# Kernel optimization log

Hardware: AMD Instinct MI355X
Metric: run time of the kernel (lower is better)

## Reference

```python
import jax, jax.numpy as jnp
import numpy as np

ANNEALING_SCALE = 0.1
BS, NV, S, D, V = 2, 16, 1024, 768, 50257

def setup_inputs() -> dict:
    key = jax.random.key(0)
    k1, k2, k3, k4, k5 = jax.random.split(key, 5)
    return {
        "input_ids": jax.random.randint(k1, (BS, S), 0, V),
        "content": jax.random.normal(k2, (BS, NV, S, D), dtype=jnp.float32),
        "contextualization": jax.random.normal(k3, (BS, NV, S, S), dtype=jnp.float32) * 0.05,
        "lm_head_weight": jax.random.normal(k4, (V, D), dtype=jnp.float32) * 0.02,
        "content_weights": jax.random.uniform(k5, (V, NV), dtype=jnp.float32),
    }

def reference(input_ids, content, contextualization, lm_head_weight, content_weights):
    bs, nv, s, d = content.shape
    # --- mask_annealing ---
    # Original computes relu(content @ W.T) over full vocab then gathers at input_ids.
    # Equivalent: gather rows of W first, then contract (same math since relu is
    # elementwise and only gathered columns are summed).
    Wg = lm_head_weight[input_ids]                              # (bs, s, d)
    sims = jnp.einsum('bkid,bjd->bkij', content, Wg)            # (bs, 16, s, s)
    sims = jnp.sum(jax.nn.relu(sims), axis=3)                   # (bs, 16, s)
    scores = jax.nn.sigmoid(-ANNEALING_SCALE * sims + 6.0)
    # upweight_nearby modifier
    scores = scores * (1.0 + jnp.arange(s, dtype=content.dtype) / 100.0)[None, None, :]
    scores = jnp.transpose(scores, (0, 2, 1))                   # (bs, s, 16)
    # --- create_content_soft_mask ---
    cw = content_weights[input_ids]                             # (bs, s, 16)
    weights = cw * scores + (1.0 - scores)                      # (bs, s, 16)
    # --- weighted sense combination ---
    content_m = content * jnp.transpose(weights, (0, 2, 1))[..., None]  # (bs,16,s,d)
    hidden = jnp.einsum('bkij,bkjd->bid', contextualization, content_m) # (bs, s, d)
    logits = hidden @ lm_head_weight.T                          # (bs, s, vocab)
    return logits
```

## Files before the change

### kernel.cpp

```cpp
#include <hip/hip_runtime.h>
#include <cstdint>
#include <cstddef>

#define BSZ 2
#define NV 16
#define SEQ 1024
#define DIM 768
#define VOC 50257
#define VOCP 50304

typedef unsigned int u32;
typedef unsigned short u16;
typedef _Float16 half8 __attribute__((ext_vector_type(8)));
typedef float f32x4 __attribute__((ext_vector_type(4)));

__device__ __forceinline__ u16 f2h(float f) {
  return __builtin_bit_cast(unsigned short, (_Float16)f);
}
__device__ __forceinline__ u32 pk2h(float a, float b) {
  return (u32)f2h(a) | ((u32)f2h(b) << 16);
}

__device__ __forceinline__ void gload16(const u16* g, u16* l) {
  __builtin_amdgcn_global_load_lds(
      (const __attribute__((address_space(1))) void*)g,
      (__attribute__((address_space(3))) void*)l, 16, 0, 0);
}

__global__ void k_prep_content(const float* __restrict__ content,
                               u16* __restrict__ cbf, u16* __restrict__ cT) {
  __shared__ u16 tile[64][70];
  const int bk = blockIdx.z;
  const int d0 = blockIdx.x * 64, j0 = blockIdx.y * 64;
  const float* src = content + (size_t)bk * SEQ * DIM;
  u16* dst = cbf + (size_t)bk * SEQ * DIM;
  u16* dstT = cT + (size_t)bk * DIM * SEQ;
  const int c4 = (threadIdx.x & 15) * 4;
  const int r0 = threadIdx.x >> 4;
#pragma unroll
  for (int it = 0; it < 4; ++it) {
    const int r = it * 16 + r0;
    const float4 f = *(const float4*)(src + (size_t)(j0 + r) * DIM + d0 + c4);
    const u32 lo = pk2h(f.x, f.y), hi = pk2h(f.z, f.w);
    *(uint2*)(dst + (size_t)(j0 + r) * DIM + d0 + c4) = make_uint2(lo, hi);
    *(u32*)&tile[r][c4] = lo;
    *(u32*)&tile[r][c4 + 2] = hi;
  }
  __syncthreads();
#pragma unroll
  for (int it = 0; it < 4; ++it) {
    const int dd = it * 16 + r0;
    const int j4 = c4;
    const u32 lo = (u32)tile[j4][dd] | ((u32)tile[j4 + 1][dd] << 16);
    const u32 hi = (u32)tile[j4 + 2][dd] | ((u32)tile[j4 + 3][dd] << 16);
    *(uint2*)(dstT + (size_t)(d0 + dd) * SEQ + j0 + j4) = make_uint2(lo, hi);
  }
}

__global__ void k_prep_w(const float* __restrict__ W, u16* __restrict__ Wb) {
  const size_t nW = (size_t)VOC * DIM / 4;
  const size_t total = (size_t)VOCP * DIM / 4;
  for (size_t u = (size_t)blockIdx.x * 256 + threadIdx.x; u < total;
       u += (size_t)gridDim.x * 256) {
    u32 lo = 0u, hi = 0u;
    if (u < nW) {
      const float4 f = *(const float4*)(W + u * 4);
      lo = pk2h(f.x, f.y); hi = pk2h(f.z, f.w);
    }
    *(uint2*)(Wb + u * 4) = make_uint2(lo, hi);
  }
}

__global__ void k_gather(const int* __restrict__ ids, const u16* __restrict__ Wb,
                         u16* __restrict__ Wg) {
  const int b = blockIdx.y, j = blockIdx.x;
  const int row = ids[b * SEQ + j];
  const int c = threadIdx.x * 4;
  *(uint2*)(Wg + ((size_t)b * SEQ + j) * DIM + c) =
      *(const uint2*)(Wb + (size_t)row * DIM + c);
}

__global__ void k_zero(float* __restrict__ p, int n) {
  const int i = blockIdx.x * 256 + threadIdx.x;
  if (i < n) p[i] = 0.f;
}

template <int LDA, int LDB>
__device__ __forceinline__ void gemm_ring2(const u16* __restrict__ A0,
                                           const u16* __restrict__ A1,
                                           const u16* __restrict__ B, int ksteps,
                                           u16* As0, u16* As1, u16* Bs,
                                           f32x4 (&acc0)[4][4],
                                           f32x4 (&acc1)[4][4], int t) {
  const int lane = t & 63, w = t >> 6, wr = w >> 1, wc = w & 1;
  const int rl = lane & 15;
  const int gsw = (((lane >> 4) ^ ((rl >> 1) & 3)) * 8);
  const int srow = 16 * w + (lane >> 2);
  const int sg = (((lane & 3) ^ ((lane >> 3) & 3)) * 8);
  const size_t gaBase = (size_t)srow * LDA + sg;
  const size_t gbBase = (size_t)srow * LDB + sg;
  const int wof = w * 512;

#define STG3_(ss, kt)                                                   \
  {                                                                     \
    const u16* ga0_ = A0 + gaBase + (size_t)(kt) * 32;                  \
    const u16* ga1_ = A1 + gaBase + (size_t)(kt) * 32;                  \
    const u16* gb_ = B + gbBase + (size_t)(kt) * 32;                    \
    gload16(ga0_, As0 + (ss) * 4096 + wof);                             \
    gload16(ga0_ + (size_t)64 * LDA, As0 + (ss) * 4096 + wof + 2048);   \
    gload16(ga1_, As1 + (ss) * 4096 + wof);                            \
    gload16(ga1_ + (size_t)64 * LDA, As1 + (ss) * 4096 + wof + 2048);   \
    gload16(gb_, Bs + (ss) * 4096 + wof);                              \
    gload16(gb_ + (size_t)64 * LDB, Bs + (ss) * 4096 + wof + 2048);     \
  }

#define FRAGS3_(ss)                                                     \
  half8 af0[4], af1[4], bf[4];                                          \
  _Pragma("unroll") for (int n = 0; n < 4; ++n)                         \
      bf[n] = *(const half8*)(Bs + (ss) * 4096 +                        \
                              (wc * 64 + n * 16 + rl) * 32 + gsw);      \
  _Pragma("unroll") for (int m = 0; m < 4; ++m)                         \
      af0[m] = *(const half8*)(As0 + (ss) * 4096 +                      \
                               (wr * 64 + m * 16 + rl) * 32 + gsw);     \
  _Pragma("unroll") for (int m = 0; m < 4; ++m)                         \
      af1[m] = *(const half8*)(As1 + (ss) * 4096 +                      \
                               (wr * 64 + m * 16 + rl) * 32 + gsw);

#define MFMA32_                                                         \
  __builtin_amdgcn_s_setprio(1);                                        \
  _Pragma("unroll") for (int m = 0; m < 4; ++m)                         \
      _Pragma("unroll") for (int n = 0; n < 4; ++n)                     \
          acc0[m][n] = __builtin_amdgcn_mfma_f32_16x16x32_f16(          \
              af0[m], bf[n], acc0[m][n], 0, 0, 0);                      \
  _Pragma("unroll") for (int m = 0; m < 4; ++m)                         \
      _Pragma("unroll") for (int n = 0; n < 4; ++n)                     \
          acc1[m][n] = __builtin_amdgcn_mfma_f32_16x16x32_f16(          \
              af1[m], bf[n], acc1[m][n], 0, 0, 0);                      \
  __builtin_amdgcn_s_setprio(0);

#define STEPF_(ss, kt)                                                  \
  asm volatile("s_waitcnt vmcnt(6)" ::: "memory");                      \
  __builtin_amdgcn_s_barrier();                                         \
  __builtin_amdgcn_sched_barrier(0);                                    \
  STG3_(((ss) + 2) % 3, (kt) + 2);                                      \
  { FRAGS3_(ss) MFMA32_ }

#define STEPL6_(ss)                                                     \
  asm volatile("s_waitcnt vmcnt(6)" ::: "memory");                      \
  __builtin_amdgcn_s_barrier();                                         \
  __builtin_amdgcn_sched_barrier(0);                                    \
  { FRAGS3_(ss) MFMA32_ }

#define STEPL0_(ss)                                                     \
  asm volatile("s_waitcnt vmcnt(0)" ::: "memory");                      \
  __builtin_amdgcn_s_barrier();                                         \
  __builtin_amdgcn_sched_barrier(0);                                    \
  { FRAGS3_(ss) MFMA32_ }

  STG3_(0, 0);
  STG3_(1, 1);
  const int nTrip = ksteps / 3;
  for (int u = 0; u < nTrip - 1; ++u) {
    const int kt = 3 * u;
    STEPF_(0, kt);
    STEPF_(1, kt + 1);
    STEPF_(2, kt + 2);
  }
  STEPF_(0, ksteps - 3);
  STEPL6_(1);
  STEPL0_(2);
#undef STG3_
#undef FRAGS3_
#undef MFMA32_
#undef STEPF_
#undef STEPL6_
#undef STEPL0_
}

__global__ __launch_bounds__(256, 2) void k_sims(const u16* __restrict__ cbf,
                                                 const u16* __restrict__ Wg,
                                                 float* __restrict__ sims) {
  __shared__ __align__(16) u16 As0[3 * 4096];
  __shared__ __align__(16) u16 As1[3 * 4096];
  __shared__ __align__(16) u16 Bs[3 * 4096];
  const int bk = blockIdx.z, b = bk >> 4;
  const int t = threadIdx.x;
  const int i0 = blockIdx.y * 256;
  const u16* A0 = cbf + (size_t)bk * SEQ * DIM + (size_t)i0 * DIM;
  const u16* A1 = A0 + (size_t)128 * DIM;
  const u16* B = Wg + (size_t)b * SEQ * DIM + (size_t)(blockIdx.x * 128) * DIM;
  f32x4 acc0[4][4] = {}, acc1[4][4] = {};
  gemm_ring2<DIM, DIM>(A0, A1, B, DIM / 32, As0, As1, Bs, acc0, acc1, t);
  const int lane = t & 63, w = t >> 6, wr = w >> 1;
  const int rg = lane >> 4, cl = lane & 15;
#pragma unroll
  for (int m = 0; m < 4; ++m) {
#pragma unroll
    for (int r = 0; r < 4; ++r) {
      float s0 = 0.f, s1 = 0.f;
#pragma unroll
      for (int n = 0; n < 4; ++n) {
        s0 += fmaxf(acc0[m][n][r], 0.f);
        s1 += fmaxf(acc1[m][n][r], 0.f);
      }
      s0 += __shfl_xor(s0, 1); s1 += __shfl_xor(s1, 1);
      s0 += __shfl_xor(s0, 2); s1 += __shfl_xor(s1, 2);
      s0 += __shfl_xor(s0, 4); s1 += __shfl_xor(s1, 4);
      s0 += __shfl_xor(s0, 8); s1 += __shfl_xor(s1, 8);
      if (cl == 0) {
        const int i = i0 + wr * 64 + m * 16 + rg * 4 + r;
        atomicAdd(&sims[(size_t)bk * SEQ + i], s0);
        atomicAdd(&sims[(size_t)bk * SEQ + i + 128], s1);
      }
    }
  }
}

__global__ void k_weights(const float* __restrict__ sims, const int* __restrict__ ids,
                          const float* __restrict__ cw, float* __restrict__ wtsT) {
  const int j = blockIdx.x * 256 + threadIdx.x;
  const int bk = blockIdx.y;
  const int b = bk >> 4, k = bk & 15;
  const float sm = sims[(size_t)bk * SEQ + j];
  float score = 1.f / (1.f + __expf(0.1f * sm - 6.f));
  score *= 1.f + (float)j * 0.01f;
  const int id = ids[b * SEQ + j];
  const float c = cw[(size_t)id * NV + k];
  wtsT[(size_t)bk * SEQ + j] = c * score + (1.f - score);
}

__global__ __launch_bounds__(256, 3) void k_hidden(const float* __restrict__ ctx,
                                                   const float* __restrict__ wtsT,
                                                   const u16* __restrict__ cT,
                                                   float* __restrict__ part) {
  __shared__ __align__(16) u16 As[2 * 4096];
  __shared__ __align__(16) u16 Bs[2 * 4096];
  const int L = blockIdx.x;
  const int g8 = L & 7, q = L >> 3;
  const int p = g8 * 16 + q / 6;
  const int dt = q % 6;
  const int y = p & 7, z = p >> 3;
  const int b = z >> 3, grp = z & 7;
  const int i0 = y * 128, d0 = dt * 128;
  const int t = threadIdx.x;
  const int lane = t & 63, w = t >> 6, wr = w >> 1, wc = w & 1;
  const int rl = lane & 15;
  const int gsw = (((lane >> 4) ^ ((rl >> 1) & 3)) * 8);
  const int srow = 16 * w + (lane >> 2);
  const int sg = (((lane & 3) ^ ((lane >> 3) & 3)) * 8);

  f32x4 acc[4][4] = {};
  float4 ra0, ra1, ra2, ra3, rw0, rw1;
  uint4 rb0, rb1;

#define LDREGS(u_)                                                      \
  {                                                                     \
    const int s_ = (u_) >> 5, kt_ = (u_) & 31;                          \
    const size_t bkq_ = (size_t)b * NV + grp * 2 + s_;                  \
    const int jsw_ = kt_ * 32 + sg;                                     \
    const float* ap_ = ctx + (bkq_ * SEQ + i0 + srow) * SEQ + jsw_;     \
    ra0 = *(const float4*)(ap_);                                        \
    ra1 = *(const float4*)(ap_ + 4);                                    \
    ra2 = *(const float4*)(ap_ + (size_t)64 * SEQ);                     \
    ra3 = *(const float4*)(ap_ + (size_t)64 * SEQ + 4);                 \
    const float* wp_ = wtsT + bkq_ * SEQ + jsw_;                        \
    rw0 = *(const float4*)(wp_);                                        \
    rw1 = *(const float4*)(wp_ + 4);                                    \
    const u16* bp_ = cT + (bkq_ * DIM + d0 + srow) * SEQ + jsw_;        \
    rb0 = *(const uint4*)(bp_);                                         \
    rb1 = *(const uint4*)(bp_ + (size_t)64 * SEQ);                      \
  }

#define WRITE(cc)                                                       \
  {                                                                     \
    u16* da_ = As + (cc) * 4096 + w * 512 + lane * 8;                   \
    *(uint4*)(da_) =                                                    \
        make_uint4(pk2h(ra0.x * rw0.x, ra0.y * rw0.y),                  \
                   pk2h(ra0.z * rw0.z, ra0.w * rw0.w),                  \
                   pk2h(ra1.x * rw1.x, ra1.y * rw1.y),                  \
                   pk2h(ra1.z * rw1.z, ra1.w * rw1.w));                 \
    *(uint4*)(da_ + 2048) =                                             \
        make_uint4(pk2h(ra2.x * rw0.x, ra2.y * rw0.y),                  \
                   pk2h(ra2.z * rw0.z, ra2.w * rw0.w),                  \
                   pk2h(ra3.x * rw1.x, ra3.y * rw1.y),                  \
                   pk2h(ra3.z * rw1.z, ra3.w * rw1.w));                 \
    u16* db_ = Bs + (cc) * 4096 + w * 512 + lane * 8;                   \
    *(uint4*)(db_) = rb0;                                               \
    *(uint4*)(db_ + 2048) = rb1;                                        \
  }

  LDREGS(0);
  int cur = 0;
#pragma unroll 1
  for (int u = 0; u < 64; ++u) {
    __syncthreads();
    WRITE(cur);
    if (u < 63) LDREGS(u + 1);
    __syncthreads();
    half8 af[4], bf[4];
#pragma unroll
    for (int m = 0; m < 4; ++m)
      af[m] = *(const half8*)(As + cur * 4096 + (wr * 64 + m * 16 + rl) * 32 + gsw);
#pragma unroll
    for (int n = 0; n < 4; ++n)
      bf[n] = *(const half8*)(Bs + cur * 4096 + (wc * 64 + n * 16 + rl) * 32 + gsw);
    __builtin_amdgcn_s_setprio(1);
#pragma unroll
    for (int m = 0; m < 4; ++m)
#pragma unroll
      for (int n = 0; n < 4; ++n)
        acc[m][n] = __builtin_amdgcn_mfma_f32_16x16x32_f16(af[m], bf[n], acc[m][n], 0, 0, 0);
    __builtin_amdgcn_s_setprio(0);
    cur ^= 1;
  }
#undef LDREGS
#undef WRITE

  const int rg = lane >> 4, cl = lane & 15;
  float* P = part + ((size_t)(grp * BSZ + b) * SEQ + i0) * DIM + d0;
#pragma unroll
  for (int m = 0; m < 4; ++m)
#pragma unroll
    for (int n = 0; n < 4; ++n)
#pragma unroll
      for (int r = 0; r < 4; ++r)
        P[(size_t)(wr * 64 + m * 16 + rg * 4 + r) * DIM + wc * 64 + n * 16 + cl] =
            acc[m][n][r];
}

__global__ void k_reduce(const float* __restrict__ part, u16* __restrict__ hid) {
  const size_t i = ((size_t)blockIdx.x * 256 + threadIdx.x) * 4;
  const size_t NHID = (size_t)BSZ * SEQ * DIM;
  float4 s = {0.f, 0.f, 0.f, 0.f};
#pragma unroll
  for (int g = 0; g < 8; ++g) {
    const float4 p = *(const float4*)(part + (size_t)g * NHID + i);
    s.x += p.x; s.y += p.y; s.z += p.z; s.w += p.w;
  }
  *(uint2*)(hid + i) = make_uint2(pk2h(s.x, s.y), pk2h(s.z, s.w));
}

__global__ __launch_bounds__(256, 2) void k_logits(const u16* __restrict__ hid,
                                                   const u16* __restrict__ Wb,
                                                   float* __restrict__ out) {
  __shared__ __align__(16) u16 lds[3 * 12288];
  const int bid = blockIdx.x;
  const int swz = (bid & 7) * 393 + (bid >> 3);
  const int it = swz & 7, vt = swz >> 3;
  const int i0 = it * 256, v0 = vt * 128;
  const int t = threadIdx.x;
  const int lane = t & 63, w = t >> 6;
  const int wm = w >> 1, wn = w & 1;
  const int rl = lane & 15, kg = lane >> 4;
  const int gsw = (kg ^ ((rl >> 1) & 3)) * 8;
  const int srow = t >> 2;
  const int sgr = ((t & 3) ^ ((srow >> 1) & 3)) * 8;
  const u16* Abase = hid + ((size_t)i0 + srow) * DIM + sgr;
  const u16* Bbase = Wb + ((size_t)v0 + srow) * DIM + sgr;
  u16* dls = lds + t * 8;

#define STG(ss, koff)                                                 \
  {                                                                   \
    const u16* a_ = Abase + (koff);                                   \
    u16* d_ = dls + (ss) * 12288;                                     \
    gload16(a_, d_);                                                  \
    gload16(a_ + (size_t)64 * DIM, d_ + 2048);                        \
    gload16(a_ + (size_t)128 * DIM, d_ + 4096);                       \
    gload16(a_ + (size_t)192 * DIM, d_ + 6144);                       \
    const u16* b_ = Bbase + (koff);                                   \
    gload16(b_, d_ + 8192);                                           \
    gload16(b_ + (size_t)64 * DIM, d_ + 10240);                       \
  }

#define CMP(ss)                                                       \
  {                                                                   \
    half8 af[8], bf[4];                                               \
    _Pragma("unroll") for (int n = 0; n < 4; ++n)                     \
        bf[n] = *(const half8*)(lds + (ss) * 12288 + 8192 +           \
                                (wn * 64 + n * 16 + rl) * 32 + gsw);  \
    _Pragma("unroll") for (int m = 0; m < 8; ++m)                     \
        af[m] = *(const half8*)(lds + (ss) * 12288 +                  \
                                (wm * 128 + m * 16 + rl) * 32 + gsw); \
    __builtin_amdgcn_s_setprio(1);                                    \
    _Pragma("unroll") for (int m = 0; m < 8; ++m)                     \
        _Pragma("unroll") for (int n = 0; n < 4; ++n)                 \
            acc[m][n] = __builtin_amdgcn_mfma_f32_16x16x32_f16(       \
                af[m], bf[n], acc[m][n], 0, 0, 0);                    \
    __builtin_amdgcn_s_setprio(0);                                    \
  }

#define BARS                                                          \
  __builtin_amdgcn_s_barrier();                                       \
  __builtin_amdgcn_sched_barrier(0);

#define STEPF(ss, st, koff)                                           \
  asm volatile("s_waitcnt vmcnt(6)" ::: "memory");                    \
  BARS;                                                               \
  STG(st, koff);                                                      \
  CMP(ss)

  f32x4 acc[8][4] = {};
  STG(0, 0);
  STG(1, 32);
#pragma unroll 1
  for (int u = 0; u < 7; ++u) {
    const int kb = u * 96;
    STEPF(0, 2, kb + 64);
    STEPF(1, 0, kb + 96);
    STEPF(2, 1, kb + 128);
  }
  STEPF(0, 2, 736);
  asm volatile("s_waitcnt vmcnt(6)" ::: "memory");
  BARS;
  CMP(1);
  asm volatile("s_waitcnt vmcnt(0)" ::: "memory");
  BARS;
  CMP(2);
#undef STG
#undef CMP
#undef BARS
#undef STEPF

#pragma unroll
  for (int m = 0; m < 8; ++m)
#pragma unroll
    for (int n = 0; n < 4; ++n) {
      const int vv = v0 + wn * 64 + n * 16 + rl;
      if (vv < VOC) {
        const int ib = i0 + wm * 128 + m * 16 + kg * 4;
#pragma unroll
        for (int r = 0; r < 4; ++r)
          out[(size_t)(ib + r) * VOC + vv] = acc[m][n][r];
      }
    }
}

extern "C" void kernel_launch(void* const* d_in, const int* in_sizes, int n_in,
                              void* d_out, int out_size, void* d_ws, size_t ws_size,
                              hipStream_t stream) {
  const int* ids = (const int*)d_in[0];
  const float* content = (const float*)d_in[1];
  const float* ctx = (const float*)d_in[2];
  const float* W = (const float*)d_in[3];
  const float* cw = (const float*)d_in[4];
  float* out = (float*)d_out;
  char* ws = (char*)d_ws;

  u16* cbf  = (u16*)(ws);
  u16* cT   = (u16*)(ws + 50331648);
  u16* Wb   = (u16*)(ws + 100663296);
  u16* Wg   = (u16*)(ws + 177930240);
  float* sims = (float*)(ws + 248184832);
  float* wtsT = (float*)(ws + 248315904);
  float* part = (float*)cbf;
  u16* hid = Wg;

  k_prep_content<<<dim3(DIM / 64, SEQ / 64, BSZ * NV), 256, 0, stream>>>(
      content, cbf, cT);
  k_prep_w<<<2048, 256, 0, stream>>>(W, Wb);
  k_gather<<<dim3(SEQ, BSZ), 192, 0, stream>>>(ids, Wb, Wg);
  k_zero<<<128, 256, 0, stream>>>(sims, BSZ * NV * SEQ);
  k_sims<<<dim3(8, 4, BSZ * NV), 256, 0, stream>>>(cbf, Wg, sims);
  k_weights<<<dim3(4, BSZ * NV), 256, 0, stream>>>(sims, ids, cw, wtsT);
  k_hidden<<<768, 256, 0, stream>>>(ctx, wtsT, cT, part);
  k_reduce<<<1536, 256, 0, stream>>>(part, hid);
  k_logits<<<8 * 393, 256, 0, stream>>>(hid, Wb, out);
}
```

Before: 549.7 us.

## Pre-pack lm_head weights into MFMA fragment order and load B directly to registers

The fp16 weight conversion now writes the vocabulary matrix in a tiled layout that matches the MFMA B-fragment order (128 vocab rows by 32 k per tile). The logits GEMM loads B fragments straight from global memory into registers, using a triple register buffer instead of staging B through LDS. This cuts LDS use and LDS read traffic for B, and the gather kernel is rewritten to index the new tiled layout. In exchange it adds more outstanding vector-memory loads per wave and more register pressure, and B reads lose any reuse they had through LDS.

```diff
diff --git a/kernel.cpp b/kernel.cpp
--- a/kernel.cpp
+++ b/kernel.cpp
@@ -26,6 +26,7 @@
       (const __attribute__((address_space(1))) void*)g,
       (__attribute__((address_space(3))) void*)l, 16, 0, 0);
 }
+
 
 __global__ void k_prep_content(const float* __restrict__ content,
                                u16* __restrict__ cbf, u16* __restrict__ cT) {
@@ -58,26 +59,38 @@
 }
 
 __global__ void k_prep_w(const float* __restrict__ W, u16* __restrict__ Wb) {
-  const size_t nW = (size_t)VOC * DIM / 4;
-  const size_t total = (size_t)VOCP * DIM / 4;
-  for (size_t u = (size_t)blockIdx.x * 256 + threadIdx.x; u < total;
-       u += (size_t)gridDim.x * 256) {
-    u32 lo = 0u, hi = 0u;
-    if (u < nW) {
-      const float4 f = *(const float4*)(W + u * 4);
-      lo = pk2h(f.x, f.y); hi = pk2h(f.z, f.w);
+  const int tile = blockIdx.x;
+  const int vb = tile / 24, ks = tile % 24;
+  const int t = threadIdx.x;
+#pragma unroll
+  for (int s = 0; s < 2; ++s) {
+    const int q = s * 256 + t;
+    const int lane = q & 63, m = q >> 6;
+    const int rl = lane & 15, kg = lane >> 4;
+    const int v = vb * 128 + m * 16 + rl;
+    const int c0 = ks * 32 + kg * 8;
+    u32 x0 = 0, x1 = 0, x2 = 0, x3 = 0;
+    if (v < VOC) {
+      const float4 f0 = *(const float4*)(W + (size_t)v * DIM + c0);
+      const float4 f1 = *(const float4*)(W + (size_t)v * DIM + c0 + 4);
+      x0 = pk2h(f0.x, f0.y); x1 = pk2h(f0.z, f0.w);
+      x2 = pk2h(f1.x, f1.y); x3 = pk2h(f1.z, f1.w);
     }
-    *(uint2*)(Wb + u * 4) = make_uint2(lo, hi);
+    *(uint4*)(Wb + (size_t)tile * 4096 + q * 8) = make_uint4(x0, x1, x2, x3);
   }
 }
 
 __global__ void k_gather(const int* __restrict__ ids, const u16* __restrict__ Wb,
                          u16* __restrict__ Wg) {
-  const int b = blockIdx.y, j = blockIdx.x;
-  const int row = ids[b * SEQ + j];
-  const int c = threadIdx.x * 4;
-  *(uint2*)(Wg + ((size_t)b * SEQ + j) * DIM + c) =
-      *(const uint2*)(Wb + (size_t)row * DIM + c);
+  const int b = blockIdx.y;
+  const int jj = blockIdx.x * 2 + (threadIdx.x >= 96 ? 1 : 0);
+  const int o = threadIdx.x % 96;
+  const int id = ids[b * SEQ + jj];
+  const int ks = o >> 2, kg = o & 3;
+  const int vb = id >> 7, m = (id >> 4) & 7, rl = id & 15;
+  const uint4 val = *(const uint4*)(Wb + (size_t)(vb * 24 + ks) * 4096 +
+                                    m * 512 + (kg * 16 + rl) * 8);
+  *(uint4*)(Wg + ((size_t)b * SEQ + jj) * DIM + o * 8) = val;
 }
 
 __global__ void k_zero(float* __restrict__ p, int n) {
@@ -341,9 +354,9 @@
 }
 
 __global__ __launch_bounds__(256, 2) void k_logits(const u16* __restrict__ hid,
-                                                   const u16* __restrict__ Wb,
+                                                   const u16* __restrict__ WbT,
                                                    float* __restrict__ out) {
-  __shared__ __align__(16) u16 lds[3 * 12288];
+  __shared__ __align__(16) u16 lds[3 * 8192];
   const int bid = blockIdx.x;
   const int swz = (bid & 7) * 393 + (bid >> 3);
   const int it = swz & 7, vt = swz >> 3;
@@ -356,36 +369,34 @@
   const int srow = t >> 2;
   const int sgr = ((t & 3) ^ ((srow >> 1) & 3)) * 8;
   const u16* Abase = hid + ((size_t)i0 + srow) * DIM + sgr;
-  const u16* Bbase = Wb + ((size_t)v0 + srow) * DIM + sgr;
+  const u16* Bt = WbT + (size_t)vt * 98304 + wn * 2048 + lane * 8;
   u16* dls = lds + t * 8;
 
-#define STG(ss, koff)                                                 \
+#define STGA(ss, koff)                                                \
   {                                                                   \
     const u16* a_ = Abase + (koff);                                   \
-    u16* d_ = dls + (ss) * 12288;                                     \
+    u16* d_ = dls + (ss) * 8192;                                      \
     gload16(a_, d_);                                                  \
     gload16(a_ + (size_t)64 * DIM, d_ + 2048);                        \
     gload16(a_ + (size_t)128 * DIM, d_ + 4096);                       \
     gload16(a_ + (size_t)192 * DIM, d_ + 6144);                       \
-    const u16* b_ = Bbase + (koff);                                   \
-    gload16(b_, d_ + 8192);                                           \
-    gload16(b_ + (size_t)64 * DIM, d_ + 10240);                       \
-  }
-
-#define CMP(ss)                                                       \
+  }
+
+#define LDB(dst, ks)                                                  \
+  _Pragma("unroll") for (int n = 0; n < 4; ++n)                       \
+      dst[n] = *(const half8*)(Bt + (size_t)(ks) * 4096 + n * 512);
+
+#define CMP(ss, bfr)                                                  \
   {                                                                   \
-    half8 af[8], bf[4];                                               \
-    _Pragma("unroll") for (int n = 0; n < 4; ++n)                     \
-        bf[n] = *(const half8*)(lds + (ss) * 12288 + 8192 +           \
-                                (wn * 64 + n * 16 + rl) * 32 + gsw);  \
+    half8 af[8];                                                      \
     _Pragma("unroll") for (int m = 0; m < 8; ++m)                     \
-        af[m] = *(const half8*)(lds + (ss) * 12288 +                  \
+        af[m] = *(const half8*)(lds + (ss) * 8192 +                   \
                                 (wm * 128 + m * 16 + rl) * 32 + gsw); \
     __builtin_amdgcn_s_setprio(1);                                    \
     _Pragma("unroll") for (int m = 0; m < 8; ++m)                     \
         _Pragma("unroll") for (int n = 0; n < 4; ++n)                 \
             acc[m][n] = __builtin_amdgcn_mfma_f32_16x16x32_f16(       \
-                af[m], bf[n], acc[m][n], 0, 0, 0);                    \
+                af[m], bfr[n], acc[m][n], 0, 0, 0);                   \
     __builtin_amdgcn_s_setprio(0);                                    \
   }
 
@@ -393,30 +404,33 @@
   __builtin_amdgcn_s_barrier();                                       \
   __builtin_amdgcn_sched_barrier(0);
 
-#define STEPF(ss, st, koff)                                           \
-  asm volatile("s_waitcnt vmcnt(6)" ::: "memory");                    \
+#define STEPF(ss, bcur, st, bnx, sk)                                  \
+  asm volatile("s_waitcnt vmcnt(8)" ::: "memory");                    \
   BARS;                                                               \
-  STG(st, koff);                                                      \
-  CMP(ss)
+  STGA(st, (sk) * 32);                                                \
+  LDB(bnx, sk);                                                       \
+  CMP(ss, bcur)
 
   f32x4 acc[8][4] = {};
-  STG(0, 0);
-  STG(1, 32);
+  half8 bA[4], bB[4], bC[4];
+  STGA(0, 0);  LDB(bA, 0);
+  STGA(1, 32); LDB(bB, 1);
 #pragma unroll 1
   for (int u = 0; u < 7; ++u) {
-    const int kb = u * 96;
-    STEPF(0, 2, kb + 64);
-    STEPF(1, 0, kb + 96);
-    STEPF(2, 1, kb + 128);
-  }
-  STEPF(0, 2, 736);
-  asm volatile("s_waitcnt vmcnt(6)" ::: "memory");
+    const int s = u * 3;
+    STEPF(0, bA, 2, bC, s + 2);
+    STEPF(1, bB, 0, bA, s + 3);
+    STEPF(2, bC, 1, bB, s + 4);
+  }
+  STEPF(0, bA, 2, bC, 23);
+  asm volatile("s_waitcnt vmcnt(8)" ::: "memory");
   BARS;
-  CMP(1);
+  CMP(1, bB);
   asm volatile("s_waitcnt vmcnt(0)" ::: "memory");
   BARS;
-  CMP(2);
-#undef STG
+  CMP(2, bC);
+#undef STGA
+#undef LDB
 #undef CMP
 #undef BARS
 #undef STEPF
@@ -457,8 +471,8 @@
 
   k_prep_content<<<dim3(DIM / 64, SEQ / 64, BSZ * NV), 256, 0, stream>>>(
       content, cbf, cT);
-  k_prep_w<<<2048, 256, 0, stream>>>(W, Wb);
-  k_gather<<<dim3(SEQ, BSZ), 192, 0, stream>>>(ids, Wb, Wg);
+  k_prep_w<<<9432, 256, 0, stream>>>(W, Wb);
+  k_gather<<<dim3(512, BSZ), 192, 0, stream>>>(ids, Wb, Wg);
   k_zero<<<128, 256, 0, stream>>>(sims, BSZ * NV * SEQ);
   k_sims<<<dim3(8, 4, BSZ * NV), 256, 0, stream>>>(cbf, Wg, sims);
   k_weights<<<dim3(4, BSZ * NV), 256, 0, stream>>>(sims, ids, cw, wtsT);
```

Result: slower. 590.9 us (+7.5%).
